# Kernel optimization log

Measured on AMD Instinct MI355X. Metric: run time of the kernel, lower is better.

The kernel has to match this reference:

```python
import jax, jax.numpy as jnp
import numpy as np

N = 200000      # total nodes
B = 1024        # graphs
D = 256         # node_dim
OUT = 256       # out_dim


def setup_inputs() -> dict:
    key = jax.random.key(0)
    ks = jax.random.split(key, 16)
    x = jax.random.normal(ks[0], (N, D), dtype=jnp.float32)
    # sorted segment ids covering all B graphs (no empty segments)
    extra = jax.random.randint(ks[1], (N - B,), 0, B)
    batch = jnp.sort(jnp.concatenate([jnp.arange(B, dtype=jnp.int32), extra.astype(jnp.int32)]))
    # one-hot node type mask [N, 3]
    types = jax.random.randint(ks[2], (N,), 0, 3)
    node_type_mask = jax.nn.one_hot(types, 3, dtype=jnp.int32)
    s = 1.0 / np.sqrt(D)
    # attn_weight: Linear(D, D//2) -> Tanh -> Linear(D//2, 1)
    aw1 = jax.random.uniform(ks[3], (D, D // 2), jnp.float32, -s, s)
    ab1 = jnp.zeros((D // 2,), jnp.float32)
    aw2 = jax.random.uniform(ks[4], (D // 2, 1), jnp.float32, -s, s)
    ab2 = jnp.zeros((1,), jnp.float32)
    # three typed transforms Linear(D, D)
    we = jax.random.uniform(ks[5], (D, D), jnp.float32, -s, s)
    be = jnp.zeros((D,), jnp.float32)
    wv = jax.random.uniform(ks[6], (D, D), jnp.float32, -s, s)
    bv = jnp.zeros((D,), jnp.float32)
    wp = jax.random.uniform(ks[7], (D, D), jnp.float32, -s, s)
    bp = jnp.zeros((D,), jnp.float32)
    # readout MLP: Linear(3D, 2*OUT) -> SiLU -> (Dropout eval) -> Linear(2*OUT, OUT)
    w1 = jax.random.uniform(ks[8], (3 * D, 2 * OUT), jnp.float32, -1.0 / np.sqrt(3 * D), 1.0 / np.sqrt(3 * D))
    b1 = jnp.zeros((2 * OUT,), jnp.float32)
    w2 = jax.random.uniform(ks[9], (2 * OUT, OUT), jnp.float32, -1.0 / np.sqrt(2 * OUT), 1.0 / np.sqrt(2 * OUT))
    b2 = jnp.zeros((OUT,), jnp.float32)
    return dict(x=x, batch=batch, node_type_mask=node_type_mask, num_segments=B,
                aw1=aw1, ab1=ab1, aw2=aw2, ab2=ab2, we=we, be=be, wv=wv, bv=bv,
                wp=wp, bp=bp, w1=w1, b1=b1, w2=w2, b2=b2)


def reference(x, batch, node_type_mask, num_segments,
              aw1, ab1, aw2, ab2, we, be, wv, bv, wp, bp, w1, b1, w2, b2):
    nseg = int(num_segments)
    # global_mean_pool
    counts = jax.ops.segment_sum(jnp.ones((x.shape[0],), x.dtype), batch, num_segments=nseg)
    mean_pool = jax.ops.segment_sum(x, batch, num_segments=nseg) / counts[:, None]
    # attention scores + segment softmax
    scores = jnp.tanh(x @ aw1 + ab1) @ aw2 + ab2            # [N, 1]
    s = scores[:, 0]
    m = jax.ops.segment_max(s, batch, num_segments=nseg)    # [B]
    e = jnp.exp(s - m[batch])
    z = jax.ops.segment_sum(e, batch, num_segments=nseg)
    attn = e / z[batch]                                     # [N]
    attn_pool = jax.ops.segment_sum(x * attn[:, None], batch, num_segments=nseg)
    # typed physical pooling (node_type_mask path)
    mask = node_type_mask.astype(x.dtype)
    typed_x = (mask[:, 0:1] * (x @ we + be)
               + mask[:, 1:2] * (x @ wv + bv)
               + mask[:, 2:3] * (x @ wp + bp))
    phys_pool = jax.ops.segment_sum(typed_x, batch, num_segments=nseg)
    combined = jnp.concatenate([mean_pool, attn_pool, phys_pool], axis=-1)  # [B, 3D]
    h = jax.nn.silu(combined @ w1 + b1)                     # dropout = identity (eval)
    return h @ w2 + b2                                      # [B, OUT]
```

## Files before the change

kernel.cpp:

```cpp
#include <hip/hip_runtime.h>

typedef float  f32x4  __attribute__((ext_vector_type(4)));
typedef short  s16x8  __attribute__((ext_vector_type(8)));
typedef short  s16x4  __attribute__((ext_vector_type(4)));

__device__ __forceinline__ short f2bf(float f) {
  unsigned u = __float_as_uint(f);
  u += 0x7fffu + ((u >> 16) & 1u);
  return (short)(u >> 16);
}
__device__ __forceinline__ float bf2f(unsigned short us) {
  return __uint_as_float(((unsigned)us) << 16);
}
__device__ __forceinline__ float tanh_fast(float x) {
  const float e = __expf(2.0f * x);
  return 1.0f - 2.0f / (e + 1.0f);
}

__global__ __launch_bounds__(256) void k_cvtw(
    const float* __restrict__ aw1, const float* __restrict__ we, const float* __restrict__ wv,
    const float* __restrict__ wp, const float* __restrict__ w1, const float* __restrict__ w2,
    unsigned short* __restrict__ Awt, unsigned short* __restrict__ Wpt,
    unsigned short* __restrict__ W1t, unsigned short* __restrict__ W2t) {
  const int b = blockIdx.x, tid = threadIdx.x;
  if (b < 128) {
    const int e = b * 256 + tid, n = e >> 8, k = e & 255;
    Awt[e] = (unsigned short)f2bf(aw1[k * 128 + n]);
  } else if (b < 896) {
    const int e = (b - 128) * 256 + tid, n = e / 768, k = e % 768;
    const int part = k >> 8, kk = k & 255;
    const float* W = (part == 0) ? we : ((part == 1) ? wv : wp);
    Wpt[e] = (unsigned short)f2bf(W[kk * 256 + n]);
  } else if (b < 2432) {
    const int e = (b - 896) * 256 + tid, n = e / 768, k = e % 768;
    W1t[e] = (unsigned short)f2bf(w1[k * 512 + n]);
  } else {
    const int e = (b - 2432) * 256 + tid, n = e >> 9, k = e & 511;
    W2t[e] = (unsigned short)f2bf(w2[k * 256 + n]);
  }
}

__global__ __launch_bounds__(256, 2) void k_score_pool(
    const float* __restrict__ x, const int* __restrict__ batch, const int* __restrict__ mask,
    const unsigned short* __restrict__ Awt, const float* __restrict__ ab1,
    const float* __restrict__ aw2, const float* __restrict__ ab2,
    float* __restrict__ P, float* __restrict__ EX, float* __restrict__ ZC,
    int nnodes) {
  __shared__ __align__(16) short xs[32][264];
  __shared__ __align__(16) short xsB[2][8192];
  __shared__ __align__(16) float sred[4][32];
  __shared__ __align__(16) short em[16][40];
  __shared__ int st_all[320];

  const int tid  = threadIdx.x;
  const int lane = tid & 63;
  const int w    = tid >> 6;
  const int quad = lane >> 4;
  const int l15  = lane & 15;

  s16x8 bfrag[8][2];
  float ab1v[2], aw2v[2];
#pragma unroll
  for (int ct = 0; ct < 2; ++ct) {
    const int col = w * 32 + ct * 16 + l15;
    ab1v[ct] = ab1[col];
    aw2v[ct] = aw2[col];
    const s16x8* bp = reinterpret_cast<const s16x8*>(Awt + (size_t)col * 256);
#pragma unroll
    for (int kt = 0; kt < 8; ++kt) bfrag[kt][ct] = bp[kt * 4 + quad];
  }
  const float ab2v = ab2[0];

  const int tiles = nnodes >> 5;
  const int t_beg = (int)(((long long)blockIdx.x * tiles) / (long long)gridDim.x);
  const int t_end = (int)(((long long)(blockIdx.x + 1) * tiles) / (long long)gridDim.x);
  if (t_beg >= t_end) return;

  {
    const int nodes0 = t_beg * 32, nblk = (t_end - t_beg) * 32;
    for (int i = tid; i < nblk; i += 256) {
      const int g = nodes0 + i;
      st_all[i] = batch[g] * 4 + mask[g * 3 + 1] + 2 * mask[g * 3 + 2];
    }
    for (int i = tid; i < 640; i += 256) (&em[0][0])[i] = 0;
  }

  f32x4 stg[8];
  auto load_regs = [&](int tile) {
    const f32x4* xp = reinterpret_cast<const f32x4*>(x + (size_t)tile * 8192);
#pragma unroll
    for (int i = 0; i < 8; ++i) stg[i] = xp[(8 * w + i) * 64 + lane];
  };
  auto cvt_write = [&](int bB) {
    s16x4 xv[8];
#pragma unroll
    for (int i = 0; i < 8; ++i) {
      xv[i][0] = f2bf(stg[i][0]); xv[i][1] = f2bf(stg[i][1]);
      xv[i][2] = f2bf(stg[i][2]); xv[i][3] = f2bf(stg[i][3]);
    }
#pragma unroll
    for (int i = 0; i < 8; ++i)
      *reinterpret_cast<s16x4*>(&xs[8 * w + i][lane * 4]) = xv[i];
    const int gb = (lane >> 2) * 4 + w;
    const int lb = (lane & 3) * 4;
#pragma unroll
    for (int q = 0; q < 4; ++q) {
      s16x8 v;
#pragma unroll
      for (int j = 0; j < 8; ++j) v[j] = xv[j][q];
      *reinterpret_cast<s16x8*>(&xsB[bB][(gb * 16 + lb + q) * 8]) = v;
    }
  };

  load_regs(t_beg);
  cvt_write(0);
  __syncthreads();

  const f32x4 zero4 = {0.f, 0.f, 0.f, 0.f};
  f32x4 accB[4] = {zero4, zero4, zero4, zero4};
  float zA = 0.f, c0A = 0.f, c1A = 0.f, c2A = 0.f;
  int cur = -1;

  auto flushB = [&]() {
#pragma unroll
    for (int c = 0; c < 4; ++c) {
      const int col = w * 64 + c * 16 + l15;
      if (quad == 0) {
        atomicAdd(&EX[cur * 256 + col], accB[c][0] + accB[c][1]);
        atomicAdd(&P[cur * 768 + col], accB[c][2]);
        atomicAdd(&P[cur * 768 + 256 + col], accB[c][3]);
      } else if (quad == 1) {
        atomicAdd(&P[cur * 768 + 512 + col], accB[c][0]);
      }
      accB[c] = zero4;
    }
    if (w == 0) {
      if (lane < 4) {
        const float v = (lane == 0) ? zA : ((lane == 1) ? c0A : ((lane == 2) ? c1A : c2A));
        atomicAdd(&ZC[cur * 4 + lane], v);
      }
      zA = c0A = c1A = c2A = 0.f;
    }
  };

  for (int tile = t_beg; tile < t_end; ++tile) {
    const int buf = (tile - t_beg) & 1;
    const bool more = (tile + 1 < t_end);
    if (more) load_regs(tile + 1);

#pragma unroll
    for (int ng = 0; ng < 2; ++ng) {
      s16x8 af[8];
#pragma unroll
      for (int kt = 0; kt < 8; ++kt)
        af[kt] = *reinterpret_cast<const s16x8*>(&xs[16 * ng + l15][kt * 32 + quad * 8]);
      float part[4] = {0.f, 0.f, 0.f, 0.f};
#pragma unroll
      for (int ct = 0; ct < 2; ++ct) {
        f32x4 acc = {0.f, 0.f, 0.f, 0.f};
#pragma unroll
        for (int kt = 0; kt < 8; ++kt)
          acc = __builtin_amdgcn_mfma_f32_16x16x32_bf16(af[kt], bfrag[kt][ct], acc, 0, 0, 0);
#pragma unroll
        for (int r = 0; r < 4; ++r)
          part[r] += tanh_fast(acc[r] + ab1v[ct]) * aw2v[ct];
      }
#pragma unroll
      for (int off = 1; off < 16; off <<= 1) {
#pragma unroll
        for (int r = 0; r < 4; ++r) part[r] += __shfl_xor(part[r], off);
      }
      if (l15 == 0) {
#pragma unroll
        for (int r = 0; r < 4; ++r) sred[w][16 * ng + quad * 4 + r] = part[r];
      }
    }
    __syncthreads();

    const int base = (tile - t_beg) * 32;

    float e_f = 0.f;
    int myt = 3;
    if (lane < 32) {
      const float s = ab2v + sred[0][lane] + sred[1][lane] + sred[2][lane] + sred[3][lane];
      e_f = __expf(s);
      const unsigned short hi = (unsigned short)f2bf(e_f);
      const unsigned short lo = (unsigned short)f2bf(e_f - bf2f(hi));
      myt = st_all[base + lane] & 3;
      em[0][lane] = (short)hi;
      em[1][lane] = (short)lo;
      em[2][lane] = (myt == 0) ? (short)0x3f80 : (short)0;
      em[3][lane] = (myt == 1) ? (short)0x3f80 : (short)0;
      em[4][lane] = (myt == 2) ? (short)0x3f80 : (short)0;
    }
    const int myseg = (lane < 32) ? (st_all[base + lane] >> 2) : 0x7fffffff;

    s16x8 emf = *reinterpret_cast<const s16x8*>(&em[l15][quad * 8]);
    s16x8 bfB[4];
#pragma unroll
    for (int c = 0; c < 4; ++c)
      bfB[c] = *reinterpret_cast<const s16x8*>(
          &xsB[buf][(((w * 4 + c) * 4 + quad) * 16 + l15) * 8]);

    int n0 = 0;
    while (n0 < 32) {
      const int seg = st_all[base + n0] >> 2;
      const unsigned long long diff = __ballot(lane < 32 && myseg != seg) >> n0;
      const int n1 = (diff == 0) ? 32 : n0 + (int)__builtin_ctzll(diff);
      if (seg != cur) { if (cur >= 0) flushB(); cur = seg; }
      s16x8 af;
      const int kb = quad * 8;
#pragma unroll
      for (int j = 0; j < 8; ++j) {
        const int k = kb + j;
        af[j] = (k >= n0 && k < n1) ? emf[j] : (short)0;
      }
#pragma unroll
      for (int c = 0; c < 4; ++c)
        accB[c] = __builtin_amdgcn_mfma_f32_16x16x32_bf16(af, bfB[c], accB[c], 0, 0, 0);
      if (w == 0) {
        const bool inrun = (lane >= n0 && lane < n1 && lane < 32);
        float ee = inrun ? e_f : 0.f;
#pragma unroll
        for (int off = 1; off < 32; off <<= 1) ee += __shfl_xor(ee, off);
        const unsigned long long b0 = __ballot(inrun && myt == 0);
        const unsigned long long b1 = __ballot(inrun && myt == 1);
        const unsigned long long b2 = __ballot(inrun && myt == 2);
        zA  += ee;
        c0A += (float)__popcll(b0);
        c1A += (float)__popcll(b1);
        c2A += (float)__popcll(b2);
      }
      n0 = n1;
    }

    if (more) cvt_write(buf ^ 1);
    __syncthreads();
  }
  if (cur >= 0) flushB();
}

__global__ __launch_bounds__(256) void k_finalize(
    const float* __restrict__ P, const float* __restrict__ EX,
    const float* __restrict__ ZC, float* __restrict__ comb) {
  const int b = blockIdx.x, d = threadIdx.x;
  const float p0 = P[b * 768 + d], p1 = P[b * 768 + 256 + d], p2 = P[b * 768 + 512 + d];
  const float cnt = ZC[b * 4 + 1] + ZC[b * 4 + 2] + ZC[b * 4 + 3];
  comb[(size_t)b * 768 + d]       = (p0 + p1 + p2) / cnt;
  comb[(size_t)b * 768 + 256 + d] = EX[b * 256 + d] / ZC[b * 4];
}

__global__ __launch_bounds__(256) void k_phys(
    const float* __restrict__ P, const unsigned short* __restrict__ Wpt,
    const float* __restrict__ be, const float* __restrict__ bv, const float* __restrict__ bp,
    const float* __restrict__ ZC, float* __restrict__ comb) {
  __shared__ __align__(16) short as16[16][776];
  const int tid = threadIdx.x, lane = tid & 63, w = tid >> 6;
  const int quad = lane >> 4, l15 = lane & 15;
  const int rowbase = blockIdx.x * 16;
  const int col = blockIdx.y * 64 + w * 16 + l15;

  s16x8 bfr[24];
  const s16x8* bpf = reinterpret_cast<const s16x8*>(Wpt + (size_t)col * 768);
#pragma unroll
  for (int kt = 0; kt < 24; ++kt) bfr[kt] = bpf[kt * 4 + quad];

  const f32x4* ap = reinterpret_cast<const f32x4*>(P + (size_t)rowbase * 768);
#pragma unroll
  for (int i = 0; i < 12; ++i) {
    const int ci = tid + 256 * i;
    f32x4 v = ap[ci];
    const int row = ci / 192, c4 = (ci % 192) * 4;
    s16x4 b; b[0] = f2bf(v[0]); b[1] = f2bf(v[1]); b[2] = f2bf(v[2]); b[3] = f2bf(v[3]);
    *reinterpret_cast<s16x4*>(&as16[row][c4]) = b;
  }
  __syncthreads();

  f32x4 acc = {0.f, 0.f, 0.f, 0.f};
#pragma unroll
  for (int kt = 0; kt < 24; ++kt) {
    s16x8 af = *reinterpret_cast<const s16x8*>(&as16[l15][kt * 32 + quad * 8]);
    acc = __builtin_amdgcn_mfma_f32_16x16x32_bf16(af, bfr[kt], acc, 0, 0, 0);
  }
  const float ben = be[col], bvn = bv[col], bpn = bp[col];
#pragma unroll
  for (int r = 0; r < 4; ++r) {
    const int row = rowbase + quad * 4 + r;
    const float v = acc[r] + ZC[row * 4 + 1] * ben + ZC[row * 4 + 2] * bvn + ZC[row * 4 + 3] * bpn;
    comb[(size_t)row * 768 + 512 + col] = v;
  }
}

__global__ __launch_bounds__(256) void k_mlp1(
    const float* __restrict__ A, const unsigned short* __restrict__ W1t,
    const float* __restrict__ b1, float* __restrict__ H) {
  __shared__ __align__(16) short as16[16][776];
  const int tid = threadIdx.x, lane = tid & 63, w = tid >> 6;
  const int quad = lane >> 4, l15 = lane & 15;
  const int rowbase = blockIdx.x * 16;
  const int col = blockIdx.y * 64 + w * 16 + l15;

  s16x8 bfr[24];
  const s16x8* bpf = reinterpret_cast<const s16x8*>(W1t + (size_t)col * 768);
#pragma unroll
  for (int kt = 0; kt < 24; ++kt) bfr[kt] = bpf[kt * 4 + quad];

  const f32x4* ap = reinterpret_cast<const f32x4*>(A + (size_t)rowbase * 768);
#pragma unroll
  for (int i = 0; i < 12; ++i) {
    const int ci = tid + 256 * i;
    f32x4 v = ap[ci];
    const int row = ci / 192, c4 = (ci % 192) * 4;
    s16x4 b; b[0] = f2bf(v[0]); b[1] = f2bf(v[1]); b[2] = f2bf(v[2]); b[3] = f2bf(v[3]);
    *reinterpret_cast<s16x4*>(&as16[row][c4]) = b;
  }
  __syncthreads();

  f32x4 acc = {0.f, 0.f, 0.f, 0.f};
#pragma unroll
  for (int kt = 0; kt < 24; ++kt) {
    s16x8 af = *reinterpret_cast<const s16x8*>(&as16[l15][kt * 32 + quad * 8]);
    acc = __builtin_amdgcn_mfma_f32_16x16x32_bf16(af, bfr[kt], acc, 0, 0, 0);
  }
  const float bn = b1[col];
#pragma unroll
  for (int r = 0; r < 4; ++r) {
    const int row = rowbase + quad * 4 + r;
    const float v = acc[r] + bn;
    H[(size_t)row * 512 + col] = v / (1.f + __expf(-v));
  }
}

__global__ __launch_bounds__(256) void k_mlp2(
    const float* __restrict__ A, const unsigned short* __restrict__ W2t,
    const float* __restrict__ b2, float* __restrict__ out) {
  __shared__ __align__(16) short as16[16][520];
  const int tid = threadIdx.x, lane = tid & 63, w = tid >> 6;
  const int quad = lane >> 4, l15 = lane & 15;
  const int rowbase = blockIdx.x * 16;
  const int col = blockIdx.y * 64 + w * 16 + l15;

  s16x8 bfr[16];
  const s16x8* bpf = reinterpret_cast<const s16x8*>(W2t + (size_t)col * 512);
#pragma unroll
  for (int kt = 0; kt < 16; ++kt) bfr[kt] = bpf[kt * 4 + quad];

  const f32x4* ap = reinterpret_cast<const f32x4*>(A + (size_t)rowbase * 512);
#pragma unroll
  for (int i = 0; i < 8; ++i) {
    const int ci = tid + 256 * i;
    f32x4 v = ap[ci];
    const int row = ci >> 7, c4 = (ci & 127) * 4;
    s16x4 b; b[0] = f2bf(v[0]); b[1] = f2bf(v[1]); b[2] = f2bf(v[2]); b[3] = f2bf(v[3]);
    *reinterpret_cast<s16x4*>(&as16[row][c4]) = b;
  }
  __syncthreads();

  f32x4 acc = {0.f, 0.f, 0.f, 0.f};
#pragma unroll
  for (int kt = 0; kt < 16; ++kt) {
    s16x8 af = *reinterpret_cast<const s16x8*>(&as16[l15][kt * 32 + quad * 8]);
    acc = __builtin_amdgcn_mfma_f32_16x16x32_bf16(af, bfr[kt], acc, 0, 0, 0);
  }
  const float bn = b2[col];
#pragma unroll
  for (int r = 0; r < 4; ++r) {
    const int row = rowbase + quad * 4 + r;
    out[(size_t)row * 256 + col] = acc[r] + bn;
  }
}

extern "C" void kernel_launch(void* const* d_in, const int* in_sizes, int n_in,
                              void* d_out, int out_size, void* d_ws, size_t ws_size,
                              hipStream_t stream) {
  const float* x    = (const float*)d_in[0];
  const int*   batch= (const int*)  d_in[1];
  const int*   mask = (const int*)  d_in[2];
  const float* aw1  = (const float*)d_in[4];
  const float* ab1  = (const float*)d_in[5];
  const float* aw2  = (const float*)d_in[6];
  const float* ab2  = (const float*)d_in[7];
  const float* we   = (const float*)d_in[8];
  const float* be   = (const float*)d_in[9];
  const float* wv   = (const float*)d_in[10];
  const float* bv   = (const float*)d_in[11];
  const float* wp   = (const float*)d_in[12];
  const float* bp   = (const float*)d_in[13];
  const float* w1   = (const float*)d_in[14];
  const float* b1   = (const float*)d_in[15];
  const float* w2   = (const float*)d_in[16];
  const float* b2   = (const float*)d_in[17];
  float* out = (float*)d_out;
  const int nn = in_sizes[1];

  float* ws = (float*)d_ws;
  float* P    = ws;
  float* EXs  = P    + 786432;
  float* ZCs  = EXs  + 262144;
  float* comb = ZCs  + 4096;
  float* hbuf = comb + 786432;
  unsigned short* Awt = (unsigned short*)(hbuf + 524288);
  unsigned short* Wpt = Awt + 32768;
  unsigned short* W1t = Wpt + 196608;
  unsigned short* W2t = W1t + 393216;

  hipMemsetAsync(P, 0, (size_t)(786432 + 262144 + 4096) * sizeof(float), stream);

  k_cvtw      <<<2944, 256, 0, stream>>>(aw1, we, wv, wp, w1, w2, Awt, Wpt, W1t, W2t);
  k_score_pool<<<1024, 256, 0, stream>>>(x, batch, mask, Awt, ab1, aw2, ab2, P, EXs, ZCs, nn);
  k_finalize  <<<1024, 256, 0, stream>>>(P, EXs, ZCs, comb);
  k_phys      <<<dim3(64, 4), 256, 0, stream>>>(P, Wpt, be, bv, bp, ZCs, comb);
  k_mlp1      <<<dim3(64, 8), 256, 0, stream>>>(comb, W1t, b1, hbuf);
  k_mlp2      <<<dim3(64, 4), 256, 0, stream>>>(hbuf, W2t, b2, out);
}
```

Measured before the change: 348.7 us.

## Tile weight transposes, fuse finalize into mlp1, single-buffer xsB for occupancy

The weight conversion kernel now transposes through a shared-memory tile, so both global reads and writes are coalesced, and it runs on far fewer blocks. The finalize kernel is removed: mean and attention normalisation are computed inside mlp1 while it stages its input, and k_phys writes to a smaller PH buffer. The score/pool kernel drops the double-buffered xsB and asks for 4 blocks per CU instead of 2 to raise occupancy. To make the single buffer safe, the xsB fragment loads move before the mid-tile barrier, which adds register pressure under the tighter launch bound.

```diff
diff --git a/kernel.cpp b/kernel.cpp
--- a/kernel.cpp
+++ b/kernel.cpp
@@ -22,32 +22,37 @@
     const float* __restrict__ wp, const float* __restrict__ w1, const float* __restrict__ w2,
     unsigned short* __restrict__ Awt, unsigned short* __restrict__ Wpt,
     unsigned short* __restrict__ W1t, unsigned short* __restrict__ W2t) {
+  __shared__ short T[64][65];
   const int b = blockIdx.x, tid = threadIdx.x;
-  if (b < 128) {
-    const int e = b * 256 + tid, n = e >> 8, k = e & 255;
-    Awt[e] = (unsigned short)f2bf(aw1[k * 128 + n]);
-  } else if (b < 896) {
-    const int e = (b - 128) * 256 + tid, n = e / 768, k = e % 768;
-    const int part = k >> 8, kk = k & 255;
-    const float* W = (part == 0) ? we : ((part == 1) ? wv : wp);
-    Wpt[e] = (unsigned short)f2bf(W[kk * 256 + n]);
-  } else if (b < 2432) {
-    const int e = (b - 896) * 256 + tid, n = e / 768, k = e % 768;
-    W1t[e] = (unsigned short)f2bf(w1[k * 512 + n]);
-  } else {
-    const int e = (b - 2432) * 256 + tid, n = e >> 9, k = e & 511;
-    W2t[e] = (unsigned short)f2bf(w2[k * 256 + n]);
-  }
-}
-
-__global__ __launch_bounds__(256, 2) void k_score_pool(
+  const float* src; unsigned short* dst;
+  int N, ds, off, t;
+  if (b < 8)        { src = aw1; dst = Awt; N = 128; ds = 256; off = 0;   t = b; }
+  else if (b < 24)  { src = we;  dst = Wpt; N = 256; ds = 768; off = 0;   t = b - 8; }
+  else if (b < 40)  { src = wv;  dst = Wpt; N = 256; ds = 768; off = 256; t = b - 24; }
+  else if (b < 56)  { src = wp;  dst = Wpt; N = 256; ds = 768; off = 512; t = b - 40; }
+  else if (b < 152) { src = w1;  dst = W1t; N = 512; ds = 768; off = 0;   t = b - 56; }
+  else              { src = w2;  dst = W2t; N = 256; ds = 512; off = 0;   t = b - 152; }
+  const int ntx = N >> 6;
+  const int kt = t / ntx;
+  const int k0 = kt * 64, n0 = (t - kt * ntx) * 64;
+  const int rl = tid >> 6, cl = tid & 63;
+#pragma unroll
+  for (int i = 0; i < 16; ++i)
+    T[cl][i * 4 + rl] = f2bf(src[(size_t)(k0 + i * 4 + rl) * N + n0 + cl]);
+  __syncthreads();
+#pragma unroll
+  for (int i = 0; i < 16; ++i)
+    dst[(size_t)(n0 + i * 4 + rl) * ds + off + k0 + cl] = (unsigned short)T[i * 4 + rl][cl];
+}
+
+__global__ __launch_bounds__(256, 4) void k_score_pool(
     const float* __restrict__ x, const int* __restrict__ batch, const int* __restrict__ mask,
     const unsigned short* __restrict__ Awt, const float* __restrict__ ab1,
     const float* __restrict__ aw2, const float* __restrict__ ab2,
     float* __restrict__ P, float* __restrict__ EX, float* __restrict__ ZC,
     int nnodes) {
   __shared__ __align__(16) short xs[32][264];
-  __shared__ __align__(16) short xsB[2][8192];
+  __shared__ __align__(16) short xsB[8192];
   __shared__ __align__(16) float sred[4][32];
   __shared__ __align__(16) short em[16][40];
   __shared__ int st_all[320];
@@ -91,7 +96,7 @@
 #pragma unroll
     for (int i = 0; i < 8; ++i) stg[i] = xp[(8 * w + i) * 64 + lane];
   };
-  auto cvt_write = [&](int bB) {
+  auto cvt_write = [&]() {
     s16x4 xv[8];
 #pragma unroll
     for (int i = 0; i < 8; ++i) {
@@ -108,12 +113,12 @@
       s16x8 v;
 #pragma unroll
       for (int j = 0; j < 8; ++j) v[j] = xv[j][q];
-      *reinterpret_cast<s16x8*>(&xsB[bB][(gb * 16 + lb + q) * 8]) = v;
+      *reinterpret_cast<s16x8*>(&xsB[(gb * 16 + lb + q) * 8]) = v;
     }
   };
 
   load_regs(t_beg);
-  cvt_write(0);
+  cvt_write();
   __syncthreads();
 
   const f32x4 zero4 = {0.f, 0.f, 0.f, 0.f};
@@ -144,7 +149,6 @@
   };
 
   for (int tile = t_beg; tile < t_end; ++tile) {
-    const int buf = (tile - t_beg) & 1;
     const bool more = (tile + 1 < t_end);
     if (more) load_regs(tile + 1);
 
@@ -175,6 +179,13 @@
         for (int r = 0; r < 4; ++r) sred[w][16 * ng + quad * 4 + r] = part[r];
       }
     }
+
+    s16x8 bfB[4];
+#pragma unroll
+    for (int c = 0; c < 4; ++c)
+      bfB[c] = *reinterpret_cast<const s16x8*>(
+          &xsB[(((w * 4 + c) * 4 + quad) * 16 + l15) * 8]);
+
     __syncthreads();
 
     const int base = (tile - t_beg) * 32;
@@ -196,11 +207,6 @@
     const int myseg = (lane < 32) ? (st_all[base + lane] >> 2) : 0x7fffffff;
 
     s16x8 emf = *reinterpret_cast<const s16x8*>(&em[l15][quad * 8]);
-    s16x8 bfB[4];
-#pragma unroll
-    for (int c = 0; c < 4; ++c)
-      bfB[c] = *reinterpret_cast<const s16x8*>(
-          &xsB[buf][(((w * 4 + c) * 4 + quad) * 16 + l15) * 8]);
 
     int n0 = 0;
     while (n0 < 32) {
@@ -234,26 +240,16 @@
       n0 = n1;
     }
 
-    if (more) cvt_write(buf ^ 1);
+    if (more) cvt_write();
     __syncthreads();
   }
   if (cur >= 0) flushB();
-}
-
-__global__ __launch_bounds__(256) void k_finalize(
-    const float* __restrict__ P, const float* __restrict__ EX,
-    const float* __restrict__ ZC, float* __restrict__ comb) {
-  const int b = blockIdx.x, d = threadIdx.x;
-  const float p0 = P[b * 768 + d], p1 = P[b * 768 + 256 + d], p2 = P[b * 768 + 512 + d];
-  const float cnt = ZC[b * 4 + 1] + ZC[b * 4 + 2] + ZC[b * 4 + 3];
-  comb[(size_t)b * 768 + d]       = (p0 + p1 + p2) / cnt;
-  comb[(size_t)b * 768 + 256 + d] = EX[b * 256 + d] / ZC[b * 4];
 }
 
 __global__ __launch_bounds__(256) void k_phys(
     const float* __restrict__ P, const unsigned short* __restrict__ Wpt,
     const float* __restrict__ be, const float* __restrict__ bv, const float* __restrict__ bp,
-    const float* __restrict__ ZC, float* __restrict__ comb) {
+    const float* __restrict__ ZC, float* __restrict__ PH) {
   __shared__ __align__(16) short as16[16][776];
   const int tid = threadIdx.x, lane = tid & 63, w = tid >> 6;
   const int quad = lane >> 4, l15 = lane & 15;
@@ -287,13 +283,15 @@
   for (int r = 0; r < 4; ++r) {
     const int row = rowbase + quad * 4 + r;
     const float v = acc[r] + ZC[row * 4 + 1] * ben + ZC[row * 4 + 2] * bvn + ZC[row * 4 + 3] * bpn;
-    comb[(size_t)row * 768 + 512 + col] = v;
+    PH[(size_t)row * 256 + col] = v;
   }
 }
 
 __global__ __launch_bounds__(256) void k_mlp1(
-    const float* __restrict__ A, const unsigned short* __restrict__ W1t,
-    const float* __restrict__ b1, float* __restrict__ H) {
+    const float* __restrict__ P, const float* __restrict__ EX,
+    const float* __restrict__ ZC, const float* __restrict__ PH,
+    const unsigned short* __restrict__ W1t, const float* __restrict__ b1,
+    float* __restrict__ H) {
   __shared__ __align__(16) short as16[16][776];
   const int tid = threadIdx.x, lane = tid & 63, w = tid >> 6;
   const int quad = lane >> 4, l15 = lane & 15;
@@ -305,14 +303,16 @@
 #pragma unroll
   for (int kt = 0; kt < 24; ++kt) bfr[kt] = bpf[kt * 4 + quad];
 
-  const f32x4* ap = reinterpret_cast<const f32x4*>(A + (size_t)rowbase * 768);
-#pragma unroll
-  for (int i = 0; i < 12; ++i) {
-    const int ci = tid + 256 * i;
-    f32x4 v = ap[ci];
-    const int row = ci / 192, c4 = (ci % 192) * 4;
-    s16x4 b; b[0] = f2bf(v[0]); b[1] = f2bf(v[1]); b[2] = f2bf(v[2]); b[3] = f2bf(v[3]);
-    *reinterpret_cast<s16x4*>(&as16[row][c4]) = b;
+#pragma unroll 4
+  for (int r = 0; r < 16; ++r) {
+    const int row = rowbase + r;
+    const float z   = ZC[row * 4 + 0];
+    const float cnt = ZC[row * 4 + 1] + ZC[row * 4 + 2] + ZC[row * 4 + 3];
+    const float mp  = (P[(size_t)row * 768 + tid] + P[(size_t)row * 768 + 256 + tid] +
+                       P[(size_t)row * 768 + 512 + tid]) / cnt;
+    as16[r][tid]       = f2bf(mp);
+    as16[r][256 + tid] = f2bf(EX[(size_t)row * 256 + tid] / z);
+    as16[r][512 + tid] = f2bf(PH[(size_t)row * 256 + tid]);
   }
   __syncthreads();
 
@@ -397,8 +397,8 @@
   float* P    = ws;
   float* EXs  = P    + 786432;
   float* ZCs  = EXs  + 262144;
-  float* comb = ZCs  + 4096;
-  float* hbuf = comb + 786432;
+  float* PH   = ZCs  + 4096;
+  float* hbuf = PH   + 262144;
   unsigned short* Awt = (unsigned short*)(hbuf + 524288);
   unsigned short* Wpt = Awt + 32768;
   unsigned short* W1t = Wpt + 196608;
@@ -406,10 +406,9 @@
 
   hipMemsetAsync(P, 0, (size_t)(786432 + 262144 + 4096) * sizeof(float), stream);
 
-  k_cvtw      <<<2944, 256, 0, stream>>>(aw1, we, wv, wp, w1, w2, Awt, Wpt, W1t, W2t);
+  k_cvtw      <<<184, 256, 0, stream>>>(aw1, we, wv, wp, w1, w2, Awt, Wpt, W1t, W2t);
   k_score_pool<<<1024, 256, 0, stream>>>(x, batch, mask, Awt, ab1, aw2, ab2, P, EXs, ZCs, nn);
-  k_finalize  <<<1024, 256, 0, stream>>>(P, EXs, ZCs, comb);
-  k_phys      <<<dim3(64, 4), 256, 0, stream>>>(P, Wpt, be, bv, bp, ZCs, comb);
-  k_mlp1      <<<dim3(64, 8), 256, 0, stream>>>(comb, W1t, b1, hbuf);
+  k_phys      <<<dim3(64, 4), 256, 0, stream>>>(P, Wpt, be, bv, bp, ZCs, PH);
+  k_mlp1      <<<dim3(64, 8), 256, 0, stream>>>(P, EXs, ZCs, PH, W1t, b1, hbuf);
   k_mlp2      <<<dim3(64, 4), 256, 0, stream>>>(hbuf, W2t, b2, out);
 }
```

Result: slower. 474.9 us (+36.2%).
